# Optimization experiments

Measured on AMD Instinct MI355X. Metric: run time of the kernel, lower is better.

The kernel has to match this reference:

```python
import jax, jax.numpy as jnp
import numpy as np

N = 768
INPUT_DIM = 128
HIDDEN = 256
HEADS = 8
HEAD_DIM = HIDDEN // HEADS  # 32
SCALE = float(np.sqrt(HEAD_DIM))


def _linear_params(key, fan_in, fan_out):
    kw, kb = jax.random.split(key)
    lim = 1.0 / np.sqrt(fan_in)
    W = jax.random.uniform(kw, (fan_in, fan_out), jnp.float32, -lim, lim)
    b = jax.random.uniform(kb, (fan_out,), jnp.float32, -lim, lim)
    return W, b


def setup_inputs() -> dict:
    key = jax.random.key(0)
    ks = jax.random.split(key, 9)
    x = jax.random.normal(ks[0], (N, INPUT_DIM), jnp.float32)
    pos = jax.random.normal(ks[1], (N, 3), jnp.float32)
    Wq, bq = _linear_params(ks[2], INPUT_DIM, HIDDEN)
    Wk, bk = _linear_params(ks[3], INPUT_DIM, HIDDEN)
    Wv, bv = _linear_params(ks[4], INPUT_DIM, HIDDEN)
    Wo, bo = _linear_params(ks[5], HIDDEN, HIDDEN)
    W1, b1 = _linear_params(ks[6], 3, HIDDEN)
    W2, b2 = _linear_params(ks[7], HIDDEN, HIDDEN)
    W3, b3 = _linear_params(ks[8], HIDDEN, HEAD_DIM)
    return dict(x=x, pos=pos, Wq=Wq, bq=bq, Wk=Wk, bk=bk, Wv=Wv, bv=bv,
                Wo=Wo, bo=bo, W1=W1, b1=b1, W2=W2, b2=b2, W3=W3, b3=b3)


def reference(x, pos, Wq, bq, Wk, bk, Wv, bv, Wo, bo, W1, b1, W2, b2, W3, b3):
    n = x.shape[0]
    Q = (x @ Wq + bq).reshape(n, HEADS, HEAD_DIM)
    K = (x @ Wk + bk).reshape(n, HEADS, HEAD_DIM)
    V = (x @ Wv + bv).reshape(n, HEADS, HEAD_DIM)

    # rel_pos[i, j] = pos[j] - pos[i], shape (N, N, 3)
    rel = pos[None, :, :] - pos[:, None, :]
    h = jax.nn.relu(rel @ W1 + b1)          # (N, N, HIDDEN)
    h = jax.nn.relu(h @ W2 + b2)            # (N, N, HIDDEN)
    enc = h @ W3 + b3                        # (N, N, HEAD_DIM)

    scores = jnp.einsum('ihd,jhd->hij', Q, K) / SCALE
    scores = scores + jnp.einsum('ihd,ijd->hij', Q, enc) / SCALE
    attn = jax.nn.softmax(scores, axis=-1)   # (H, N, N); dropout is identity at eval
    out = jnp.einsum('hij,jhd->ihd', attn, V).reshape(n, HIDDEN)
    return out @ Wo + bo
```

## Files before the change

kernel.cpp:

```cpp
#include <hip/hip_runtime.h>
#include <hip/hip_bf16.h>

#define N 768
#define IN_DIM 128
#define HID 256
#define HD 32
#define TJ 64
#define NT (N / TJ)
#define SCALE_INV 0.17677669529663687f

typedef short s16x8 __attribute__((ext_vector_type(8)));
typedef float f32x4 __attribute__((ext_vector_type(4)));

__device__ __forceinline__ unsigned short bf_bits(float f) {
    __hip_bfloat16 h = __float2bfloat16(f);
    union { __hip_bfloat16 h; unsigned short u; } c; c.h = h; return c.u;
}
__device__ __forceinline__ unsigned cvt2(float a, float b) {
    __hip_bfloat162 h2 = __float22bfloat162_rn(make_float2(a, b));
    union { __hip_bfloat162 h; unsigned u; } c; c.h = h2; return c.u;
}

#define BAR_LDS() do { asm volatile("s_waitcnt lgkmcnt(0)" ::: "memory"); \
                       __builtin_amdgcn_s_barrier(); } while (0)

__global__ __launch_bounds__(256) void prep_kernel(
    const float* __restrict__ x, const float* __restrict__ pos,
    const float* __restrict__ Wq, const float* __restrict__ bq,
    const float* __restrict__ Wk, const float* __restrict__ bk,
    const float* __restrict__ Wv, const float* __restrict__ bv,
    const float* __restrict__ W1, const float* __restrict__ W2,
    const float* __restrict__ W3, const float* __restrict__ Wo,
    float* __restrict__ Q, float* __restrict__ Kt,
    float* __restrict__ Vt, float* __restrict__ A,
    unsigned short* __restrict__ w2tf, float* __restrict__ WoT,
    unsigned short* __restrict__ w3qg)
{
    const int bx = blockIdx.x, t = threadIdx.x;
    __shared__ float xs[IN_DIM];
    __shared__ float ps[3];
    __shared__ float qrow[HID];

    if (bx >= N) {
        const int p = (bx - N) * 256 + t;
        const int e = p & 7, l = (p >> 3) & 63, s = (p >> 9) & 7, kt = p >> 12;
        const int krow = 32 * s + 8 * (l >> 4) + e;
        const int kcol = 16 * kt + (l & 15);
        w2tf[p] = bf_bits(W2[krow * HID + kcol]);
        WoT[p] = Wo[(p & 255) * HID + (p >> 8)];
        return;
    }

    const int i = bx;
    if (t < IN_DIM) xs[t] = x[i * IN_DIM + t];
    if (t < 3) ps[t] = pos[i * 3 + t];
    __syncthreads();
    float q = bq[t], k = bk[t], v = bv[t];
#pragma unroll 8
    for (int kk = 0; kk < IN_DIM; ++kk) {
        const float xv = xs[kk];
        q += xv * Wq[kk * HID + t];
        k += xv * Wk[kk * HID + t];
        v += xv * Wv[kk * HID + t];
    }
    const float a = ps[0] * W1[t] + ps[1] * W1[HID + t] + ps[2] * W1[2 * HID + t];
    Q[i * HID + t] = q;
    Kt[(size_t)t * N + i] = k;
    Vt[(size_t)t * N + i] = v;
    A[i * HID + t] = a;
    qrow[t] = q;
    __syncthreads();

    const int l = t & 63, sp = t >> 6, lg = l >> 4, hh = l & 15;
#pragma unroll
    for (int ss = 0; ss < 2; ++ss) {
        const int s = 2 * sp + ss;
        s16x8 frag = {0, 0, 0, 0, 0, 0, 0, 0};
        if (hh < 8) {
#pragma unroll
            for (int e = 0; e < 8; ++e) {
                const int kk = 32 * s + 8 * lg + e;
                const float* w3p = W3 + kk * HD;
                float acc = 0.f;
#pragma unroll
                for (int d0 = 0; d0 < 32; d0 += 4) {
                    const float4 wv = *(const float4*)(w3p + d0);
                    acc += wv.x * qrow[hh * HD + d0] + wv.y * qrow[hh * HD + d0 + 1]
                         + wv.z * qrow[hh * HD + d0 + 2] + wv.w * qrow[hh * HD + d0 + 3];
                }
                frag[e] = (short)bf_bits(acc);
            }
        }
        *(s16x8*)(w3qg + (size_t)i * 4096 + (size_t)(s * 64 + l) * 8) = frag;
    }
}

__global__ __launch_bounds__(256) void s1_kernel(
    const float* __restrict__ Q, const float* __restrict__ Kt,
    float* __restrict__ S1)
{
    const int t = threadIdx.x;
    const int i0 = (blockIdx.x / 12) * 32;
    const int j0 = (blockIdx.x % 12) * 64;
    __shared__ float qTs[256 * 36];

    {
        const int iq = t & 31;
        const int dbase = (t >> 5) * 32;
        const int xk = t >> 5;
        const int colsw = (((iq >> 2) ^ xk) << 2) + (iq & 3);
        const float* qp = Q + (size_t)(i0 + iq) * HID + dbase;
#pragma unroll
        for (int cc = 0; cc < 8; ++cc) {
            const float4 qv = *(const float4*)(qp + 4 * cc);
            qTs[(dbase + 4 * cc + 0) * 36 + colsw] = qv.x;
            qTs[(dbase + 4 * cc + 1) * 36 + colsw] = qv.y;
            qTs[(dbase + 4 * cc + 2) * 36 + colsw] = qv.z;
            qTs[(dbase + 4 * cc + 3) * 36 + colsw] = qv.w;
        }
    }
    __syncthreads();

    const int h = t >> 5, jj = t & 31;
    const int j1 = j0 + jj, j2 = j0 + jj + 32;
    f32x4 acc0[8] = {}, acc1[8] = {};
    const float* kp = Kt + (size_t)(32 * h) * N + j1;
#pragma unroll 4
    for (int d = 0; d < 32; ++d) {
        const float k0 = kp[(size_t)d * N];
        const float k1 = kp[(size_t)d * N + 32];
        const float* qrow = &qTs[(32 * h + d) * 36];
#pragma unroll
        for (int ic = 0; ic < 8; ++ic) {
            const f32x4 qv = *(const f32x4*)&qrow[(ic ^ h) << 2];
            acc0[ic] += qv * k0;
            acc1[ic] += qv * k1;
        }
    }
    float* op = S1 + (size_t)h * (N * N) + (size_t)i0 * N;
#pragma unroll
    for (int ic = 0; ic < 8; ++ic)
#pragma unroll
        for (int u = 0; u < 4; ++u) {
            op[(size_t)(4 * ic + u) * N + j1] = acc0[ic][u];
            op[(size_t)(4 * ic + u) * N + j2] = acc1[ic][u];
        }
}

__global__ __launch_bounds__(256, 2) void fused_main_kernel(
    const float* __restrict__ Ag, const float* __restrict__ S1,
    const float* __restrict__ Vt,
    const unsigned short* __restrict__ w2tf, const unsigned short* __restrict__ w3qg,
    const float* __restrict__ b1, const float* __restrict__ b2,
    const float* __restrict__ WoT, const float* __restrict__ bo,
    float* __restrict__ out)
{
    const int i = blockIdx.x, t = threadIdx.x;
    const int w = t >> 6, l = t & 63;
    const int lg = l >> 4, l15 = l & 15;

    __shared__ __align__(16) short h1f[4 * 8 * 64 * 8];
    __shared__ __align__(16) short h2s[64 * 264];
    __shared__ __align__(16) short w3qf[8 * 64 * 8];
    __shared__ __align__(16) float slds[8 * 68];
    __shared__ float basek[HID];
    __shared__ float b2s[HID];
    float* const oa = slds;

    basek[t] = b1[t] - Ag[(size_t)i * HID + t];
    b2s[t] = b2[t];
    {
        const int c0 = t, c1 = t + 256;
        *(s16x8*)&w3qf[c0 * 8] = *(const s16x8*)(w3qg + (size_t)i * 4096 + (size_t)c0 * 8);
        *(s16x8*)&w3qf[c1 * 8] = *(const s16x8*)(w3qg + (size_t)i * 4096 + (size_t)c1 * 8);
    }
    float pv = 0.f, psum0 = 0.f, psum1 = 0.f;
    float mr0 = -3.0e38f, mr1 = -3.0e38f;
    const int h = t >> 5;
    __syncthreads();

#pragma unroll 1
    for (int tile = 0; tile < NT; ++tile) {
        const int j0 = tile * TJ;

        const int jj = 16 * w + l15;
        const float* ap = Ag + (size_t)(j0 + jj) * HID + 8 * lg;
#pragma unroll
        for (int s = 0; s < 8; ++s) {
            const float4 a0 = *(const float4*)(ap + 32 * s);
            const float4 a1 = *(const float4*)(ap + 32 * s + 4);
            const float4 c0 = *(const float4*)&basek[32 * s + 8 * lg];
            const float4 c4 = *(const float4*)&basek[32 * s + 8 * lg + 4];
            uint4 hv;
            hv.x = cvt2(fmaxf(a0.x + c0.x, 0.f), fmaxf(a0.y + c0.y, 0.f));
            hv.y = cvt2(fmaxf(a0.z + c0.z, 0.f), fmaxf(a0.w + c0.w, 0.f));
            hv.z = cvt2(fmaxf(a1.x + c4.x, 0.f), fmaxf(a1.y + c4.y, 0.f));
            hv.w = cvt2(fmaxf(a1.z + c4.z, 0.f), fmaxf(a1.w + c4.w, 0.f));
            *(uint4*)&h1f[((w * 8 + s) * 64 + l) * 8] = hv;
        }
        float4 s1v = make_float4(0.f, 0.f, 0.f, 0.f);
        if (l15 < 8)
            s1v = *(const float4*)(S1 + (size_t)l15 * (N * N) + (size_t)i * N
                                   + j0 + 16 * w + 4 * lg);
        s16x8 bfr[32];
#pragma unroll
        for (int s = 0; s < 8; ++s)
#pragma unroll
            for (int ktl = 0; ktl < 4; ++ktl)
                bfr[s * 4 + ktl] = *(const s16x8*)(w2tf +
                    (size_t)((((4 * w + ktl) * 8 + s) * 64 + l)) * 8);
        BAR_LDS();

#pragma unroll
        for (int jjb = 0; jjb < 4; ++jjb) {
            f32x4 acc[4] = {};
#pragma unroll
            for (int s = 0; s < 8; ++s) {
                const s16x8 bfrag = *(const s16x8*)&h1f[((jjb * 8 + s) * 64 + l) * 8];
#pragma unroll
                for (int ktl = 0; ktl < 4; ++ktl)
                    acc[ktl] = __builtin_amdgcn_mfma_f32_16x16x32_bf16(
                        bfr[s * 4 + ktl], bfrag, acc[ktl], 0, 0, 0);
            }
#pragma unroll
            for (int ktl = 0; ktl < 4; ++ktl) {
                const int k0 = 64 * w + 16 * ktl + 4 * lg;
                const float4 bv = *(const float4*)&b2s[k0];
                const f32x4 a = acc[ktl];
                uint2 pw;
                pw.x = cvt2(fmaxf(a[0] + bv.x, 0.f), fmaxf(a[1] + bv.y, 0.f));
                pw.y = cvt2(fmaxf(a[2] + bv.z, 0.f), fmaxf(a[3] + bv.w, 0.f));
                *(uint2*)&h2s[(16 * jjb + l15) * 264 + k0] = pw;
            }
        }
        BAR_LDS();

        f32x4 acc2 = {};
        const int rowc = (16 * w + l15) * 264;
#pragma unroll
        for (int s = 0; s < 8; ++s) {
            const s16x8 a2 = *(const s16x8*)&h2s[rowc + 32 * s + 8 * lg];
            const s16x8 wq = *(const s16x8*)&w3qf[(s * 64 + l) * 8];
            acc2 = __builtin_amdgcn_mfma_f32_16x16x32_bf16(a2, wq, acc2, 0, 0, 0);
        }
        if (l15 < 8) {
            float4 sc;
            sc.x = (acc2[0] + s1v.x) * SCALE_INV;
            sc.y = (acc2[1] + s1v.y) * SCALE_INV;
            sc.z = (acc2[2] + s1v.z) * SCALE_INV;
            sc.w = (acc2[3] + s1v.w) * SCALE_INV;
            *(float4*)&slds[l15 * 68 + 16 * w + 4 * lg] = sc;
        }
        BAR_LDS();

        {
            const int h0 = 2 * w, h1 = 2 * w + 1;
            const float s0 = slds[h0 * 68 + l];
            const float s1 = slds[h1 * 68 + l];
            float m0 = s0, m1 = s1;
#pragma unroll
            for (int o = 1; o < 64; o <<= 1) {
                m0 = fmaxf(m0, __shfl_xor(m0, o));
                m1 = fmaxf(m1, __shfl_xor(m1, o));
            }
            const float nm0 = fmaxf(mr0, m0), nm1 = fmaxf(mr1, m1);
            const float r0 = __expf(mr0 - nm0), r1 = __expf(mr1 - nm1);
            mr0 = nm0; mr1 = nm1;
            const float p0 = __expf(s0 - nm0), p1 = __expf(s1 - nm1);
            psum0 = psum0 * r0 + p0;
            psum1 = psum1 * r1 + p1;
            slds[h0 * 68 + l] = p0;
            slds[h1 * 68 + l] = p1;
            asm volatile("s_waitcnt lgkmcnt(0)" ::: "memory");
            pv *= (l < 32) ? r0 : r1;
            const float* vp = Vt + (size_t)t * N + j0;
            const float* pp = &slds[h * 68];
#pragma unroll
            for (int cc = 0; cc < 4; ++cc) {
                const float4 v0 = *(const float4*)(vp + 16 * cc);
                const float4 v1 = *(const float4*)(vp + 16 * cc + 4);
                const float4 v2 = *(const float4*)(vp + 16 * cc + 8);
                const float4 v3 = *(const float4*)(vp + 16 * cc + 12);
                const float4 pa = *(const float4*)(pp + 16 * cc);
                const float4 pb = *(const float4*)(pp + 16 * cc + 4);
                const float4 pc = *(const float4*)(pp + 16 * cc + 8);
                const float4 pd = *(const float4*)(pp + 16 * cc + 12);
                pv += pa.x * v0.x + pa.y * v0.y + pa.z * v0.z + pa.w * v0.w
                    + pb.x * v1.x + pb.y * v1.y + pb.z * v1.z + pb.w * v1.w
                    + pc.x * v2.x + pc.y * v2.y + pc.z * v2.z + pc.w * v2.w
                    + pd.x * v3.x + pd.y * v3.y + pd.z * v3.z + pd.w * v3.w;
            }
        }
    }

#pragma unroll
    for (int o = 1; o < 64; o <<= 1) {
        psum0 += __shfl_xor(psum0, o);
        psum1 += __shfl_xor(psum1, o);
    }
    const float denom = (l < 32) ? psum0 : psum1;
    __syncthreads();
    oa[t] = pv / denom;
    __syncthreads();
    float r = bo[t];
    const float* wop = WoT + (size_t)t * HID;
#pragma unroll 4
    for (int k = 0; k < HID; k += 4) {
        const float4 ov = *(const float4*)&oa[k];
        const float4 wv = *(const float4*)(wop + k);
        r += ov.x * wv.x + ov.y * wv.y + ov.z * wv.z + ov.w * wv.w;
    }
    out[(size_t)i * HID + t] = r;
}

extern "C" void kernel_launch(void* const* d_in, const int* in_sizes, int n_in,
                              void* d_out, int out_size, void* d_ws, size_t ws_size,
                              hipStream_t stream)
{
    const float* x   = (const float*)d_in[0];
    const float* pos = (const float*)d_in[1];
    const float* Wq  = (const float*)d_in[2];
    const float* bq  = (const float*)d_in[3];
    const float* Wk  = (const float*)d_in[4];
    const float* bk  = (const float*)d_in[5];
    const float* Wv  = (const float*)d_in[6];
    const float* bv  = (const float*)d_in[7];
    const float* Wo  = (const float*)d_in[8];
    const float* bo  = (const float*)d_in[9];
    const float* W1  = (const float*)d_in[10];
    const float* b1  = (const float*)d_in[11];
    const float* W2  = (const float*)d_in[12];
    const float* b2  = (const float*)d_in[13];
    const float* W3  = (const float*)d_in[14];
    const float* b3  = (const float*)d_in[15];
    (void)b3;
    float* out = (float*)d_out;

    char* ws = (char*)d_ws;
    float* Q  = (float*)(ws + 0);
    float* A  = (float*)(ws + 786432);
    float* Kt = (float*)(ws + 1572864);
    float* Vt = (float*)(ws + 2359296);
    float* S1 = (float*)(ws + 3145728);
    unsigned short* w2tf = (unsigned short*)(ws + 22020096);
    unsigned short* w3qg = (unsigned short*)(ws + 22151168);
    float* WoT = (float*)(ws + 28442624);

    prep_kernel<<<1024, 256, 0, stream>>>(x, pos, Wq, bq, Wk, bk, Wv, bv,
                                          W1, W2, W3, Wo,
                                          Q, Kt, Vt, A, w2tf, WoT, w3qg);
    s1_kernel<<<288, 256, 0, stream>>>(Q, Kt, S1);
    fused_main_kernel<<<N, 256, 0, stream>>>(A, S1, Vt, w2tf, w3qg,
                                             b1, b2, WoT, bo, out);
}
```

Baseline: 237.4 us.

## Halve j-tile to 32 and raise occupancy to three blocks per CU

Shrinks the per-iteration key tile from 64 to 32 columns, cutting the LDS buffers roughly in half. The launch bound goes from 2 to 3 blocks per CU so more waves can hide latency. The work split is reorganised: the h1 build is spread over all four waves, only two waves run the W3 projection, and softmax now handles one head per 32-lane half-wave. The cost is twice as many tile iterations and barriers, idle waves in the W3 stage, and fewer registers per thread, which risks spilling the 32-entry bfr array.

```diff
diff --git a/kernel.cpp b/kernel.cpp
--- a/kernel.cpp
+++ b/kernel.cpp
@@ -5,7 +5,7 @@
 #define IN_DIM 128
 #define HID 256
 #define HD 32
-#define TJ 64
+#define TJ 32
 #define NT (N / TJ)
 #define SCALE_INV 0.17677669529663687f
 
@@ -147,7 +147,7 @@
         }
 }
 
-__global__ __launch_bounds__(256, 2) void fused_main_kernel(
+__global__ __launch_bounds__(256, 3) void fused_main_kernel(
     const float* __restrict__ Ag, const float* __restrict__ S1,
     const float* __restrict__ Vt,
     const unsigned short* __restrict__ w2tf, const unsigned short* __restrict__ w3qg,
@@ -159,10 +159,10 @@
     const int w = t >> 6, l = t & 63;
     const int lg = l >> 4, l15 = l & 15;
 
-    __shared__ __align__(16) short h1f[4 * 8 * 64 * 8];
-    __shared__ __align__(16) short h2s[64 * 264];
+    __shared__ __align__(16) short h1f[2 * 8 * 64 * 8];
+    __shared__ __align__(16) short h2s[32 * 264];
     __shared__ __align__(16) short w3qf[8 * 64 * 8];
-    __shared__ __align__(16) float slds[8 * 68];
+    __shared__ __align__(16) float slds[8 * 36];
     __shared__ float basek[HID];
     __shared__ float b2s[HID];
     float* const oa = slds;
@@ -174,32 +174,38 @@
         *(s16x8*)&w3qf[c0 * 8] = *(const s16x8*)(w3qg + (size_t)i * 4096 + (size_t)c0 * 8);
         *(s16x8*)&w3qf[c1 * 8] = *(const s16x8*)(w3qg + (size_t)i * 4096 + (size_t)c1 * 8);
     }
-    float pv = 0.f, psum0 = 0.f, psum1 = 0.f;
-    float mr0 = -3.0e38f, mr1 = -3.0e38f;
-    const int h = t >> 5;
+    float pv = 0.f, psum = 0.f, mr = -3.0e38f;
+    const int head = t >> 5;
+    const int jj32 = l & 31;
+    const int jjb_a = w & 1;
+    const int sb_a = (w >> 1) * 4;
     __syncthreads();
 
 #pragma unroll 1
     for (int tile = 0; tile < NT; ++tile) {
         const int j0 = tile * TJ;
 
-        const int jj = 16 * w + l15;
-        const float* ap = Ag + (size_t)(j0 + jj) * HID + 8 * lg;
-#pragma unroll
-        for (int s = 0; s < 8; ++s) {
-            const float4 a0 = *(const float4*)(ap + 32 * s);
-            const float4 a1 = *(const float4*)(ap + 32 * s + 4);
-            const float4 c0 = *(const float4*)&basek[32 * s + 8 * lg];
-            const float4 c4 = *(const float4*)&basek[32 * s + 8 * lg + 4];
-            uint4 hv;
-            hv.x = cvt2(fmaxf(a0.x + c0.x, 0.f), fmaxf(a0.y + c0.y, 0.f));
-            hv.y = cvt2(fmaxf(a0.z + c0.z, 0.f), fmaxf(a0.w + c0.w, 0.f));
-            hv.z = cvt2(fmaxf(a1.x + c4.x, 0.f), fmaxf(a1.y + c4.y, 0.f));
-            hv.w = cvt2(fmaxf(a1.z + c4.z, 0.f), fmaxf(a1.w + c4.w, 0.f));
-            *(uint4*)&h1f[((w * 8 + s) * 64 + l) * 8] = hv;
+        {
+            const int jj = 16 * jjb_a + l15;
+            const float* ap = Ag + (size_t)(j0 + jj) * HID;
+#pragma unroll
+            for (int ss = 0; ss < 4; ++ss) {
+                const int s = sb_a + ss;
+                const int k0 = 32 * s + 8 * lg;
+                const float4 a0 = *(const float4*)(ap + k0);
+                const float4 a1 = *(const float4*)(ap + k0 + 4);
+                const float4 c0 = *(const float4*)&basek[k0];
+                const float4 c4 = *(const float4*)&basek[k0 + 4];
+                uint4 hv;
+                hv.x = cvt2(fmaxf(a0.x + c0.x, 0.f), fmaxf(a0.y + c0.y, 0.f));
+                hv.y = cvt2(fmaxf(a0.z + c0.z, 0.f), fmaxf(a0.w + c0.w, 0.f));
+                hv.z = cvt2(fmaxf(a1.x + c4.x, 0.f), fmaxf(a1.y + c4.y, 0.f));
+                hv.w = cvt2(fmaxf(a1.z + c4.z, 0.f), fmaxf(a1.w + c4.w, 0.f));
+                *(uint4*)&h1f[((jjb_a * 8 + s) * 64 + l) * 8] = hv;
+            }
         }
         float4 s1v = make_float4(0.f, 0.f, 0.f, 0.f);
-        if (l15 < 8)
+        if (w < 2 && l15 < 8)
             s1v = *(const float4*)(S1 + (size_t)l15 * (N * N) + (size_t)i * N
                                    + j0 + 16 * w + 4 * lg);
         s16x8 bfr[32];
@@ -212,7 +218,7 @@
         BAR_LDS();
 
 #pragma unroll
-        for (int jjb = 0; jjb < 4; ++jjb) {
+        for (int jjb = 0; jjb < 2; ++jjb) {
             f32x4 acc[4] = {};
 #pragma unroll
             for (int s = 0; s < 8; ++s) {
@@ -235,48 +241,43 @@
         }
         BAR_LDS();
 
-        f32x4 acc2 = {};
-        const int rowc = (16 * w + l15) * 264;
-#pragma unroll
-        for (int s = 0; s < 8; ++s) {
-            const s16x8 a2 = *(const s16x8*)&h2s[rowc + 32 * s + 8 * lg];
-            const s16x8 wq = *(const s16x8*)&w3qf[(s * 64 + l) * 8];
-            acc2 = __builtin_amdgcn_mfma_f32_16x16x32_bf16(a2, wq, acc2, 0, 0, 0);
-        }
-        if (l15 < 8) {
-            float4 sc;
-            sc.x = (acc2[0] + s1v.x) * SCALE_INV;
-            sc.y = (acc2[1] + s1v.y) * SCALE_INV;
-            sc.z = (acc2[2] + s1v.z) * SCALE_INV;
-            sc.w = (acc2[3] + s1v.w) * SCALE_INV;
-            *(float4*)&slds[l15 * 68 + 16 * w + 4 * lg] = sc;
+        if (w < 2) {
+            f32x4 acc2 = {};
+            const int rowc = (16 * w + l15) * 264;
+#pragma unroll
+            for (int s = 0; s < 8; ++s) {
+                const s16x8 a2 = *(const s16x8*)&h2s[rowc + 32 * s + 8 * lg];
+                const s16x8 wq = *(const s16x8*)&w3qf[(s * 64 + l) * 8];
+                acc2 = __builtin_amdgcn_mfma_f32_16x16x32_bf16(a2, wq, acc2, 0, 0, 0);
+            }
+            if (l15 < 8) {
+                float4 sc;
+                sc.x = (acc2[0] + s1v.x) * SCALE_INV;
+                sc.y = (acc2[1] + s1v.y) * SCALE_INV;
+                sc.z = (acc2[2] + s1v.z) * SCALE_INV;
+                sc.w = (acc2[3] + s1v.w) * SCALE_INV;
+                *(float4*)&slds[l15 * 36 + 16 * w + 4 * lg] = sc;
+            }
         }
         BAR_LDS();
 
         {
-            const int h0 = 2 * w, h1 = 2 * w + 1;
-            const float s0 = slds[h0 * 68 + l];
-            const float s1 = slds[h1 * 68 + l];
-            float m0 = s0, m1 = s1;
-#pragma unroll
-            for (int o = 1; o < 64; o <<= 1) {
-                m0 = fmaxf(m0, __shfl_xor(m0, o));
-                m1 = fmaxf(m1, __shfl_xor(m1, o));
-            }
-            const float nm0 = fmaxf(mr0, m0), nm1 = fmaxf(mr1, m1);
-            const float r0 = __expf(mr0 - nm0), r1 = __expf(mr1 - nm1);
-            mr0 = nm0; mr1 = nm1;
-            const float p0 = __expf(s0 - nm0), p1 = __expf(s1 - nm1);
-            psum0 = psum0 * r0 + p0;
-            psum1 = psum1 * r1 + p1;
-            slds[h0 * 68 + l] = p0;
-            slds[h1 * 68 + l] = p1;
+            const float s0 = slds[head * 36 + jj32];
+            float m0 = s0;
+#pragma unroll
+            for (int o = 1; o < 32; o <<= 1) m0 = fmaxf(m0, __shfl_xor(m0, o));
+            const float nm = fmaxf(mr, m0);
+            const float r = __expf(mr - nm);
+            mr = nm;
+            const float p = __expf(s0 - nm);
+            psum = psum * r + p;
+            slds[head * 36 + jj32] = p;
             asm volatile("s_waitcnt lgkmcnt(0)" ::: "memory");
-            pv *= (l < 32) ? r0 : r1;
+            pv *= r;
             const float* vp = Vt + (size_t)t * N + j0;
-            const float* pp = &slds[h * 68];
-#pragma unroll
-            for (int cc = 0; cc < 4; ++cc) {
+            const float* pp = &slds[head * 36];
+#pragma unroll
+            for (int cc = 0; cc < 2; ++cc) {
                 const float4 v0 = *(const float4*)(vp + 16 * cc);
                 const float4 v1 = *(const float4*)(vp + 16 * cc + 4);
                 const float4 v2 = *(const float4*)(vp + 16 * cc + 8);
@@ -294,13 +295,9 @@
     }
 
 #pragma unroll
-    for (int o = 1; o < 64; o <<= 1) {
-        psum0 += __shfl_xor(psum0, o);
-        psum1 += __shfl_xor(psum1, o);
-    }
-    const float denom = (l < 32) ? psum0 : psum1;
-    __syncthreads();
-    oa[t] = pv / denom;
+    for (int o = 1; o < 32; o <<= 1) psum += __shfl_xor(psum, o);
+    __syncthreads();
+    oa[t] = pv / psum;
     __syncthreads();
     float r = bo[t];
     const float* wop = WoT + (size_t)t * HID;
```

Measured after the change: 645.3 us. +171.8%, slower.

## Software-pipeline next tile's h1, S1 and W2 fragment loads across tiles

Applied to the files above, without the earlier changes.

Moves the next tile's work to the middle of the current tile, right after the layer-2 barrier. That work is the global loads of the pairwise Ag rows, the bias-add/ReLU/bf16 conversion into h1f, the S1 bias fetch and the W2 fragment reload. This lets global memory latency overlap with the layer-3 MFMA, softmax and PV phases of the current tile, and removes one barrier per tile. The first tile is prologued before the loop. The cost is that the 32 bfr fragment registers and the prefetched values stay live through the softmax/PV phase, which raises VGPR pressure and may lower occupancy or cause spills.

```diff
diff --git a/kernel.cpp b/kernel.cpp
--- a/kernel.cpp
+++ b/kernel.cpp
@@ -177,14 +177,11 @@
     float pv = 0.f, psum0 = 0.f, psum1 = 0.f;
     float mr0 = -3.0e38f, mr1 = -3.0e38f;
     const int h = t >> 5;
-    __syncthreads();
-
-#pragma unroll 1
-    for (int tile = 0; tile < NT; ++tile) {
-        const int j0 = tile * TJ;
-
-        const int jj = 16 * w + l15;
-        const float* ap = Ag + (size_t)(j0 + jj) * HID + 8 * lg;
+    const int jjA = 16 * w + l15;
+    __syncthreads();
+
+    {
+        const float* ap = Ag + (size_t)jjA * HID + 8 * lg;
 #pragma unroll
         for (int s = 0; s < 8; ++s) {
             const float4 a0 = *(const float4*)(ap + 32 * s);
@@ -198,19 +195,22 @@
             hv.w = cvt2(fmaxf(a1.z + c4.z, 0.f), fmaxf(a1.w + c4.w, 0.f));
             *(uint4*)&h1f[((w * 8 + s) * 64 + l) * 8] = hv;
         }
-        float4 s1v = make_float4(0.f, 0.f, 0.f, 0.f);
-        if (l15 < 8)
-            s1v = *(const float4*)(S1 + (size_t)l15 * (N * N) + (size_t)i * N
-                                   + j0 + 16 * w + 4 * lg);
-        s16x8 bfr[32];
-#pragma unroll
-        for (int s = 0; s < 8; ++s)
-#pragma unroll
-            for (int ktl = 0; ktl < 4; ++ktl)
-                bfr[s * 4 + ktl] = *(const s16x8*)(w2tf +
-                    (size_t)((((4 * w + ktl) * 8 + s) * 64 + l)) * 8);
-        BAR_LDS();
-
+    }
+    s16x8 bfr[32];
+#pragma unroll
+    for (int s = 0; s < 8; ++s)
+#pragma unroll
+        for (int ktl = 0; ktl < 4; ++ktl)
+            bfr[s * 4 + ktl] = *(const s16x8*)(w2tf +
+                (size_t)((((4 * w + ktl) * 8 + s) * 64 + l)) * 8);
+    float4 s1v = make_float4(0.f, 0.f, 0.f, 0.f);
+    if (l15 < 8)
+        s1v = *(const float4*)(S1 + (size_t)l15 * (N * N) + (size_t)i * N
+                               + 16 * w + 4 * lg);
+    BAR_LDS();
+
+#pragma unroll 1
+    for (int tile = 0; tile < NT; ++tile) {
 #pragma unroll
         for (int jjb = 0; jjb < 4; ++jjb) {
             f32x4 acc[4] = {};
@@ -234,6 +234,34 @@
             }
         }
         BAR_LDS();
+
+        float4 s1v_n = make_float4(0.f, 0.f, 0.f, 0.f);
+        if (tile + 1 < NT) {
+            const int j0n = (tile + 1) * TJ;
+            const float* ap = Ag + (size_t)(j0n + jjA) * HID + 8 * lg;
+#pragma unroll
+            for (int s = 0; s < 8; ++s) {
+                const float4 a0 = *(const float4*)(ap + 32 * s);
+                const float4 a1 = *(const float4*)(ap + 32 * s + 4);
+                const float4 c0 = *(const float4*)&basek[32 * s + 8 * lg];
+                const float4 c4 = *(const float4*)&basek[32 * s + 8 * lg + 4];
+                uint4 hv;
+                hv.x = cvt2(fmaxf(a0.x + c0.x, 0.f), fmaxf(a0.y + c0.y, 0.f));
+                hv.y = cvt2(fmaxf(a0.z + c0.z, 0.f), fmaxf(a0.w + c0.w, 0.f));
+                hv.z = cvt2(fmaxf(a1.x + c4.x, 0.f), fmaxf(a1.y + c4.y, 0.f));
+                hv.w = cvt2(fmaxf(a1.z + c4.z, 0.f), fmaxf(a1.w + c4.w, 0.f));
+                *(uint4*)&h1f[((w * 8 + s) * 64 + l) * 8] = hv;
+            }
+            if (l15 < 8)
+                s1v_n = *(const float4*)(S1 + (size_t)l15 * (N * N) + (size_t)i * N
+                                         + j0n + 16 * w + 4 * lg);
+#pragma unroll
+            for (int s = 0; s < 8; ++s)
+#pragma unroll
+                for (int ktl = 0; ktl < 4; ++ktl)
+                    bfr[s * 4 + ktl] = *(const s16x8*)(w2tf +
+                        (size_t)((((4 * w + ktl) * 8 + s) * 64 + l)) * 8);
+        }
 
         f32x4 acc2 = {};
         const int rowc = (16 * w + l15) * 264;
@@ -273,7 +301,7 @@
             slds[h1 * 68 + l] = p1;
             asm volatile("s_waitcnt lgkmcnt(0)" ::: "memory");
             pv *= (l < 32) ? r0 : r1;
-            const float* vp = Vt + (size_t)t * N + j0;
+            const float* vp = Vt + (size_t)t * N + tile * TJ;
             const float* pp = &slds[h * 68];
 #pragma unroll
             for (int cc = 0; cc < 4; ++cc) {
@@ -291,6 +319,7 @@
                     + pd.x * v3.x + pd.y * v3.y + pd.z * v3.z + pd.w * v3.w;
             }
         }
+        s1v = s1v_n;
     }
 
 #pragma unroll
```

Result: slower. 374.4 us (+57.7%).

## Store V as bf16, swap MFMA operand roles, and share softmax stats per head

Applied to the files above, without the earlier changes.

V is now written in bf16 and read as 8-element vectors in the PV accumulation, halving its global traffic. The W2 fragment layout is reorganised so h1 tiles become the A operand, with b2 folded into the accumulator init. Online-softmax max, sum and rescale are moved into shared memory per head, with a separate probability buffer and an extra barrier. The head-to-wave mapping also changes. This adds synchronisation and scalar LDS stores of h2, and bf16 V slightly reduces precision.

```diff
diff --git a/kernel.cpp b/kernel.cpp
--- a/kernel.cpp
+++ b/kernel.cpp
@@ -12,6 +12,9 @@
 typedef short s16x8 __attribute__((ext_vector_type(8)));
 typedef float f32x4 __attribute__((ext_vector_type(4)));
 
+__device__ __forceinline__ float bf2f(unsigned short s) {
+    return __uint_as_float(((unsigned)s) << 16);
+}
 __device__ __forceinline__ unsigned short bf_bits(float f) {
     __hip_bfloat16 h = __float2bfloat16(f);
     union { __hip_bfloat16 h; unsigned short u; } c; c.h = h; return c.u;
@@ -32,8 +35,8 @@
     const float* __restrict__ W1, const float* __restrict__ W2,
     const float* __restrict__ W3, const float* __restrict__ Wo,
     float* __restrict__ Q, float* __restrict__ Kt,
-    float* __restrict__ Vt, float* __restrict__ A,
-    unsigned short* __restrict__ w2tf, float* __restrict__ WoT,
+    unsigned short* __restrict__ Vt, float* __restrict__ A,
+    unsigned short* __restrict__ w2f, float* __restrict__ WoT,
     unsigned short* __restrict__ w3qg)
 {
     const int bx = blockIdx.x, t = threadIdx.x;
@@ -43,10 +46,10 @@
 
     if (bx >= N) {
         const int p = (bx - N) * 256 + t;
-        const int e = p & 7, l = (p >> 3) & 63, s = (p >> 9) & 7, kt = p >> 12;
+        const int e = p & 7, l = (p >> 3) & 63, nt = (p >> 9) & 15, s = p >> 13;
         const int krow = 32 * s + 8 * (l >> 4) + e;
-        const int kcol = 16 * kt + (l & 15);
-        w2tf[p] = bf_bits(W2[krow * HID + kcol]);
+        const int ncol = 16 * nt + (l & 15);
+        w2f[p] = bf_bits(W2[krow * HID + ncol]);
         WoT[p] = Wo[(p & 255) * HID + (p >> 8)];
         return;
     }
@@ -66,7 +69,7 @@
     const float a = ps[0] * W1[t] + ps[1] * W1[HID + t] + ps[2] * W1[2 * HID + t];
     Q[i * HID + t] = q;
     Kt[(size_t)t * N + i] = k;
-    Vt[(size_t)t * N + i] = v;
+    Vt[(size_t)t * N + i] = bf_bits(v);
     A[i * HID + t] = a;
     qrow[t] = q;
     __syncthreads();
@@ -149,8 +152,8 @@
 
 __global__ __launch_bounds__(256, 2) void fused_main_kernel(
     const float* __restrict__ Ag, const float* __restrict__ S1,
-    const float* __restrict__ Vt,
-    const unsigned short* __restrict__ w2tf, const unsigned short* __restrict__ w3qg,
+    const unsigned short* __restrict__ Vt,
+    const unsigned short* __restrict__ w2fg, const unsigned short* __restrict__ w3qg,
     const float* __restrict__ b1, const float* __restrict__ b2,
     const float* __restrict__ WoT, const float* __restrict__ bo,
     float* __restrict__ out)
@@ -163,21 +166,26 @@
     __shared__ __align__(16) short h2s[64 * 264];
     __shared__ __align__(16) short w3qf[8 * 64 * 8];
     __shared__ __align__(16) float slds[8 * 68];
+    __shared__ __align__(16) float plds[8 * 68];
     __shared__ float basek[HID];
-    __shared__ float b2s[HID];
-    float* const oa = slds;
+    __shared__ float oa[HID];
+    __shared__ float hm[8], hpsum[8], hresc[8];
 
     basek[t] = b1[t] - Ag[(size_t)i * HID + t];
-    b2s[t] = b2[t];
     {
         const int c0 = t, c1 = t + 256;
         *(s16x8*)&w3qf[c0 * 8] = *(const s16x8*)(w3qg + (size_t)i * 4096 + (size_t)c0 * 8);
         *(s16x8*)&w3qf[c1 * 8] = *(const s16x8*)(w3qg + (size_t)i * 4096 + (size_t)c1 * 8);
     }
-    float pv = 0.f, psum0 = 0.f, psum1 = 0.f;
-    float mr0 = -3.0e38f, mr1 = -3.0e38f;
+    if (t < 8) { hm[t] = -3.0e38f; hpsum[t] = 0.f; }
+    float bias[4];
+#pragma unroll
+    for (int n = 0; n < 4; ++n) bias[n] = b2[64 * w + 16 * n + l15];
+
+    float pv = 0.f;
     const int h = t >> 5;
-    __syncthreads();
+    const unsigned short* vrow = Vt + (size_t)t * N;
+    BAR_LDS();
 
 #pragma unroll 1
     for (int tile = 0; tile < NT; ++tile) {
@@ -198,48 +206,44 @@
             hv.w = cvt2(fmaxf(a1.z + c4.z, 0.f), fmaxf(a1.w + c4.w, 0.f));
             *(uint4*)&h1f[((w * 8 + s) * 64 + l) * 8] = hv;
         }
+        s16x8 bfr[32];
+#pragma unroll
+        for (int s = 0; s < 8; ++s)
+#pragma unroll
+            for (int n = 0; n < 4; ++n)
+                bfr[s * 4 + n] = *(const s16x8*)(w2fg +
+                    (size_t)(((s * 16 + 4 * w + n) * 64 + l)) * 8);
+        BAR_LDS();
+
+#pragma unroll
+        for (int mt = 0; mt < 4; ++mt) {
+            s16x8 a[8];
+#pragma unroll
+            for (int s = 0; s < 8; ++s)
+                a[s] = *(const s16x8*)&h1f[((mt * 8 + s) * 64 + l) * 8];
+#pragma unroll
+            for (int n = 0; n < 4; ++n) {
+                f32x4 acc = {bias[n], bias[n], bias[n], bias[n]};
+#pragma unroll
+                for (int s = 0; s < 8; ++s)
+                    acc = __builtin_amdgcn_mfma_f32_16x16x32_bf16(a[s], bfr[s * 4 + n], acc, 0, 0, 0);
+                const int col = 64 * w + 16 * n + l15;
+                const int jrow = 16 * mt + 4 * lg;
+#pragma unroll
+                for (int r = 0; r < 4; ++r)
+                    h2s[(jrow + r) * 264 + col] = (short)bf_bits(fmaxf(acc[r], 0.f));
+            }
+        }
+        BAR_LDS();
+
         float4 s1v = make_float4(0.f, 0.f, 0.f, 0.f);
         if (l15 < 8)
             s1v = *(const float4*)(S1 + (size_t)l15 * (N * N) + (size_t)i * N
                                    + j0 + 16 * w + 4 * lg);
-        s16x8 bfr[32];
-#pragma unroll
-        for (int s = 0; s < 8; ++s)
-#pragma unroll
-            for (int ktl = 0; ktl < 4; ++ktl)
-                bfr[s * 4 + ktl] = *(const s16x8*)(w2tf +
-                    (size_t)((((4 * w + ktl) * 8 + s) * 64 + l)) * 8);
-        BAR_LDS();
-
-#pragma unroll
-        for (int jjb = 0; jjb < 4; ++jjb) {
-            f32x4 acc[4] = {};
-#pragma unroll
-            for (int s = 0; s < 8; ++s) {
-                const s16x8 bfrag = *(const s16x8*)&h1f[((jjb * 8 + s) * 64 + l) * 8];
-#pragma unroll
-                for (int ktl = 0; ktl < 4; ++ktl)
-                    acc[ktl] = __builtin_amdgcn_mfma_f32_16x16x32_bf16(
-                        bfr[s * 4 + ktl], bfrag, acc[ktl], 0, 0, 0);
-            }
-#pragma unroll
-            for (int ktl = 0; ktl < 4; ++ktl) {
-                const int k0 = 64 * w + 16 * ktl + 4 * lg;
-                const float4 bv = *(const float4*)&b2s[k0];
-                const f32x4 a = acc[ktl];
-                uint2 pw;
-                pw.x = cvt2(fmaxf(a[0] + bv.x, 0.f), fmaxf(a[1] + bv.y, 0.f));
-                pw.y = cvt2(fmaxf(a[2] + bv.z, 0.f), fmaxf(a[3] + bv.w, 0.f));
-                *(uint2*)&h2s[(16 * jjb + l15) * 264 + k0] = pw;
-            }
-        }
-        BAR_LDS();
-
         f32x4 acc2 = {};
-        const int rowc = (16 * w + l15) * 264;
 #pragma unroll
         for (int s = 0; s < 8; ++s) {
-            const s16x8 a2 = *(const s16x8*)&h2s[rowc + 32 * s + 8 * lg];
+            const s16x8 a2 = *(const s16x8*)&h2s[(16 * w + l15) * 264 + 32 * s + 8 * lg];
             const s16x8 wq = *(const s16x8*)&w3qf[(s * 64 + l) * 8];
             acc2 = __builtin_amdgcn_mfma_f32_16x16x32_bf16(a2, wq, acc2, 0, 0, 0);
         }
@@ -254,7 +258,7 @@
         BAR_LDS();
 
         {
-            const int h0 = 2 * w, h1 = 2 * w + 1;
+            const int h0 = w, h1 = w + 4;
             const float s0 = slds[h0 * 68 + l];
             const float s1 = slds[h1 * 68 + l];
             float m0 = s0, m1 = s1;
@@ -263,45 +267,46 @@
                 m0 = fmaxf(m0, __shfl_xor(m0, o));
                 m1 = fmaxf(m1, __shfl_xor(m1, o));
             }
-            const float nm0 = fmaxf(mr0, m0), nm1 = fmaxf(mr1, m1);
-            const float r0 = __expf(mr0 - nm0), r1 = __expf(mr1 - nm1);
-            mr0 = nm0; mr1 = nm1;
+            const float M0 = hm[h0], M1 = hm[h1];
+            const float nm0 = fmaxf(M0, m0), nm1 = fmaxf(M1, m1);
             const float p0 = __expf(s0 - nm0), p1 = __expf(s1 - nm1);
-            psum0 = psum0 * r0 + p0;
-            psum1 = psum1 * r1 + p1;
-            slds[h0 * 68 + l] = p0;
-            slds[h1 * 68 + l] = p1;
-            asm volatile("s_waitcnt lgkmcnt(0)" ::: "memory");
-            pv *= (l < 32) ? r0 : r1;
-            const float* vp = Vt + (size_t)t * N + j0;
-            const float* pp = &slds[h * 68];
-#pragma unroll
-            for (int cc = 0; cc < 4; ++cc) {
-                const float4 v0 = *(const float4*)(vp + 16 * cc);
-                const float4 v1 = *(const float4*)(vp + 16 * cc + 4);
-                const float4 v2 = *(const float4*)(vp + 16 * cc + 8);
-                const float4 v3 = *(const float4*)(vp + 16 * cc + 12);
-                const float4 pa = *(const float4*)(pp + 16 * cc);
-                const float4 pb = *(const float4*)(pp + 16 * cc + 4);
-                const float4 pc = *(const float4*)(pp + 16 * cc + 8);
-                const float4 pd = *(const float4*)(pp + 16 * cc + 12);
-                pv += pa.x * v0.x + pa.y * v0.y + pa.z * v0.z + pa.w * v0.w
-                    + pb.x * v1.x + pb.y * v1.y + pb.z * v1.z + pb.w * v1.w
-                    + pc.x * v2.x + pc.y * v2.y + pc.z * v2.z + pc.w * v2.w
-                    + pd.x * v3.x + pd.y * v3.y + pd.z * v3.z + pd.w * v3.w;
-            }
-        }
-    }
-
-#pragma unroll
-    for (int o = 1; o < 64; o <<= 1) {
-        psum0 += __shfl_xor(psum0, o);
-        psum1 += __shfl_xor(psum1, o);
-    }
-    const float denom = (l < 32) ? psum0 : psum1;
-    __syncthreads();
-    oa[t] = pv / denom;
-    __syncthreads();
+            plds[h0 * 68 + l] = p0;
+            plds[h1 * 68 + l] = p1;
+            float t0 = p0, t1 = p1;
+#pragma unroll
+            for (int o = 1; o < 64; o <<= 1) {
+                t0 += __shfl_xor(t0, o);
+                t1 += __shfl_xor(t1, o);
+            }
+            if (l == 0) {
+                const float r0 = __expf(M0 - nm0), r1 = __expf(M1 - nm1);
+                hresc[h0] = r0; hresc[h1] = r1;
+                hpsum[h0] = hpsum[h0] * r0 + t0;
+                hpsum[h1] = hpsum[h1] * r1 + t1;
+                hm[h0] = nm0; hm[h1] = nm1;
+            }
+        }
+        BAR_LDS();
+
+        {
+            pv *= hresc[h];
+            const unsigned short* vp = vrow + j0;
+            const float* pp = &plds[h * 68];
+#pragma unroll
+            for (int c = 0; c < 8; ++c) {
+                const s16x8 vv = *(const s16x8*)(vp + c * 8);
+                const float4 pa = *(const float4*)(pp + 8 * c);
+                const float4 pb = *(const float4*)(pp + 8 * c + 4);
+                pv += pa.x * bf2f((unsigned short)vv[0]) + pa.y * bf2f((unsigned short)vv[1])
+                    + pa.z * bf2f((unsigned short)vv[2]) + pa.w * bf2f((unsigned short)vv[3])
+                    + pb.x * bf2f((unsigned short)vv[4]) + pb.y * bf2f((unsigned short)vv[5])
+                    + pb.z * bf2f((unsigned short)vv[6]) + pb.w * bf2f((unsigned short)vv[7]);
+            }
+        }
+    }
+
+    oa[t] = pv / hpsum[h];
+    BAR_LDS();
     float r = bo[t];
     const float* wop = WoT + (size_t)t * HID;
 #pragma unroll 4
@@ -340,16 +345,16 @@
     float* Q  = (float*)(ws + 0);
     float* A  = (float*)(ws + 786432);
     float* Kt = (float*)(ws + 1572864);
-    float* Vt = (float*)(ws + 2359296);
-    float* S1 = (float*)(ws + 3145728);
-    unsigned short* w2tf = (unsigned short*)(ws + 22020096);
-    unsigned short* w3qg = (unsigned short*)(ws + 22151168);
-    float* WoT = (float*)(ws + 28442624);
+    unsigned short* Vtb = (unsigned short*)(ws + 2359296);
+    float* S1 = (float*)(ws + 2752512);
+    unsigned short* w2f  = (unsigned short*)(ws + 21626880);
+    unsigned short* w3qg = (unsigned short*)(ws + 21757952);
+    float* WoT = (float*)(ws + 28049408);
 
     prep_kernel<<<1024, 256, 0, stream>>>(x, pos, Wq, bq, Wk, bk, Wv, bv,
                                           W1, W2, W3, Wo,
-                                          Q, Kt, Vt, A, w2tf, WoT, w3qg);
+                                          Q, Kt, Vtb, A, w2f, WoT, w3qg);
     s1_kernel<<<288, 256, 0, stream>>>(Q, Kt, S1);
-    fused_main_kernel<<<N, 256, 0, stream>>>(A, S1, Vt, w2tf, w3qg,
+    fused_main_kernel<<<N, 256, 0, stream>>>(A, S1, Vtb, w2f, w3qg,
                                              b1, b2, WoT, bo, out);
 }
```

Result: faster. 227.7 us, median of 2 (-4.1%).
